# Performance work log

Hardware: AMD Instinct MI355X
Metric: run time of the kernel (lower is better)

Reference implementation:

```python
import jax, jax.numpy as jnp
import numpy as np

N = 100000   # nodes
E = 1600000  # edges
B = 256      # graphs
EPS = 1e-5   # batchnorm eps


def setup_inputs() -> dict:
    key = jax.random.key(0)
    ks = jax.random.split(key, 20)
    inp = {
        "x": jax.random.normal(ks[0], (N, 22), dtype=jnp.float32),
        "edge_index": jax.random.randint(ks[1], (2, E), 0, N, dtype=jnp.int64),
        "batch": jnp.sort(jax.random.randint(ks[2], (N,), 0, B, dtype=jnp.int64)),
        # GCNConv weights (x @ W + b convention)
        "W1": jax.random.normal(ks[3], (22, 64), dtype=jnp.float32) * 0.2,
        "b1": jnp.zeros((64,), dtype=jnp.float32),
        "W2": jax.random.normal(ks[4], (64, 64), dtype=jnp.float32) * 0.12,
        "b2": jnp.zeros((64,), dtype=jnp.float32),
        "W3": jax.random.normal(ks[5], (64, 128), dtype=jnp.float32) * 0.12,
        "b3": jnp.zeros((128,), dtype=jnp.float32),
        # BatchNorm1d params + running stats (eval mode)
        "g1": jax.random.uniform(ks[6], (64,), minval=0.5, maxval=1.5),
        "be1": jax.random.normal(ks[7], (64,)) * 0.1,
        "m1": jax.random.normal(ks[8], (64,)) * 0.1,
        "v1": jax.random.uniform(ks[9], (64,), minval=0.5, maxval=1.5),
        "g2": jax.random.uniform(ks[10], (64,), minval=0.5, maxval=1.5),
        "be2": jax.random.normal(ks[11], (64,)) * 0.1,
        "m2": jax.random.normal(ks[12], (64,)) * 0.1,
        "v2": jax.random.uniform(ks[13], (64,), minval=0.5, maxval=1.5),
    }
    return inp


def _gcn_conv(h, W, b, src, dst, norm_e, dinv):
    # PyG GCNConv: h' = D^{-1/2}(A+I)D^{-1/2} (h W) + b
    h = h @ W                                             # [N, F]
    msg = h[src] * norm_e[:, None]                        # gather + scale [E, F]
    agg = jax.ops.segment_sum(msg, dst, num_segments=N)   # scatter-add
    agg = agg + h * dinv[:, None]                         # self-loop term
    return agg + b


def _bn_eval(x, g, be, m, v):
    return (x - m) * jax.lax.rsqrt(v + EPS) * g + be


def reference(x, edge_index, batch, W1, b1, W2, b2, W3, b3,
              g1, be1, m1, v1, g2, be2, m2, v2):
    src, dst = edge_index[0], edge_index[1]
    # degree with self-loops (computed on target nodes, symmetric norm)
    deg = jax.ops.segment_sum(jnp.ones((E,), x.dtype), dst, num_segments=N) + 1.0
    dis = jax.lax.rsqrt(deg)            # deg^{-1/2}, deg >= 1
    norm_e = dis[src] * dis[dst]        # per-edge norm
    dinv = dis * dis                    # 1/deg for self-loop edges

    h = jax.nn.relu(_bn_eval(_gcn_conv(x, W1, b1, src, dst, norm_e, dinv), g1, be1, m1, v1))
    h = jax.nn.relu(_bn_eval(_gcn_conv(h, W2, b2, src, dst, norm_e, dinv), g2, be2, m2, v2))
    h = jax.nn.relu(_gcn_conv(h, W3, b3, src, dst, norm_e, dinv))

    # global mean pool over graph ids
    sums = jax.ops.segment_sum(h, batch, num_segments=B)              # [B, 128]
    cnts = jax.ops.segment_sum(jnp.ones((N,), h.dtype), batch, num_segments=B)
    return sums / jnp.maximum(cnts, 1.0)[:, None]
```

## Files before the change

### kernel.cpp

```cpp
#include <hip/hip_runtime.h>

#define BN_EPS 1e-5f

typedef _Float16 half_t;
typedef _Float16 half4 __attribute__((ext_vector_type(4)));
typedef _Float16 half8 __attribute__((ext_vector_type(8)));
typedef unsigned int u32;
typedef unsigned short u16;

__device__ __forceinline__ float norm_of(u32 w) {
    u16 hb = (u16)(w & 0x7fffu);
    return (float)__builtin_bit_cast(half_t, hb);
}


#define EPB 4096

__global__ void k_bhist(const int* __restrict__ dst, int* __restrict__ countsT,
                        int nblk, int e) {
    __shared__ int h[256];
    h[threadIdx.x] = 0;
    __syncthreads();
    int base = blockIdx.x * EPB;
    int end = min(base + EPB, e);
    for (int i = base + threadIdx.x; i < end; i += 256)
        atomicAdd(&h[dst[i] >> 9], 1);
    __syncthreads();
    countsT[threadIdx.x * nblk + blockIdx.x] = h[threadIdx.x];
}

__global__ void k_colscan(int* __restrict__ countsT, int* __restrict__ colSum, int nblk) {
    __shared__ int lds[256];
    int t = threadIdx.x;
    int* col = countsT + (size_t)blockIdx.x * nblk;
    int carry = 0;
    for (int base = 0; base < nblk; base += 512) {
        int i0 = base + t * 2, i1 = i0 + 1;
        int v0 = (i0 < nblk) ? col[i0] : 0;
        int v1 = (i1 < nblk) ? col[i1] : 0;
        int s = v0 + v1;
        int val = s;
        lds[t] = val;
        __syncthreads();
        for (int off = 1; off < 256; off <<= 1) {
            int tmp = (t >= off) ? lds[t - off] : 0;
            __syncthreads();
            val += tmp;
            lds[t] = val;
            __syncthreads();
        }
        int run = carry + val - s;
        if (i0 < nblk) col[i0] = run;
        if (i1 < nblk) col[i1] = run + v0;
        carry += lds[255];
        __syncthreads();
    }
    if (t == 0) colSum[blockIdx.x] = carry;
}

__global__ void k_bscatter(const int* __restrict__ src, const int* __restrict__ dst,
                           const int* __restrict__ countsT, const int* __restrict__ colSum,
                           u32* __restrict__ rec, int nblk, int e) {
    __shared__ int lds[256];
    __shared__ int cur[256];
    int t = threadIdx.x;
    int s = colSum[t];
    int val = s;
    lds[t] = val;
    __syncthreads();
    for (int off = 1; off < 256; off <<= 1) {
        int tmp = (t >= off) ? lds[t - off] : 0;
        __syncthreads();
        val += tmp;
        lds[t] = val;
        __syncthreads();
    }
    int basev = val - s;
    cur[t] = countsT[t * nblk + blockIdx.x] + basev;
    __syncthreads();
    int base = blockIdx.x * EPB;
    int end = min(base + EPB, e);
    for (int i = base + t; i < end; i += 256) {
        int d = dst[i], sv = src[i];
        int pos = atomicAdd(&cur[d >> 9], 1);
        rec[pos] = ((u32)sv << 9) | (u32)(d & 511);
    }
}

__global__ void k_bmake1(const u32* __restrict__ rec, const int* __restrict__ colSum,
                         int* __restrict__ rowptr, float* __restrict__ dis,
                         float* __restrict__ dinv, int n) {
    __shared__ int h[512];
    __shared__ int ps[256];
    int t = threadIdx.x;
    int cs = colSum[t];
    int val = cs;
    ps[t] = val;
    __syncthreads();
    for (int off = 1; off < 256; off <<= 1) {
        int tmp = (t >= off) ? ps[t - off] : 0;
        __syncthreads();
        val += tmp;
        ps[t] = val;
        __syncthreads();
    }
    int beg = (blockIdx.x == 0) ? 0 : ps[blockIdx.x - 1];
    int end = ps[blockIdx.x];
    __syncthreads();
    h[t] = 0; h[t + 256] = 0;
    __syncthreads();
    for (int i = beg + t; i < end; i += 256)
        atomicAdd(&h[rec[i] & 511], 1);
    __syncthreads();
    int node0 = blockIdx.x << 9;
    int d0 = h[2 * t], d1 = h[2 * t + 1];
    int pair = d0 + d1;
    ps[t] = pair;
    __syncthreads();
    int val2 = pair;
    for (int off = 1; off < 256; off <<= 1) {
        int tmp = (t >= off) ? ps[t - off] : 0;
        __syncthreads();
        val2 += tmp;
        ps[t] = val2;
        __syncthreads();
    }
    int excl0 = beg + val2 - pair;
    int nodeA = node0 + 2 * t, nodeB = nodeA + 1;
    if (nodeA <= n) rowptr[nodeA] = excl0;
    if (nodeB <= n) rowptr[nodeB] = excl0 + d0;
    if (nodeA < n) { float dd = (float)(d0 + 1); dis[nodeA] = rsqrtf(dd); dinv[nodeA] = 1.0f / dd; }
    if (nodeB < n) { float dd = (float)(d1 + 1); dis[nodeB] = rsqrtf(dd); dinv[nodeB] = 1.0f / dd; }
    if ((n & 511) == 0 && blockIdx.x == gridDim.x - 1 && t == 255) rowptr[n] = end;
}

__global__ void k_bfill(const u32* __restrict__ rec, const int* __restrict__ colSum,
                        const int* __restrict__ rowptr, const float* __restrict__ dis,
                        u32* __restrict__ csr, int n) {
    __shared__ int ps[256];
    __shared__ int cur[512];
    __shared__ float disl[512];
    int t = threadIdx.x;
    int cs = colSum[t];
    int val = cs;
    ps[t] = val;
    __syncthreads();
    for (int off = 1; off < 256; off <<= 1) {
        int tmp = (t >= off) ? ps[t - off] : 0;
        __syncthreads();
        val += tmp;
        ps[t] = val;
        __syncthreads();
    }
    int beg = (blockIdx.x == 0) ? 0 : ps[blockIdx.x - 1];
    int end = ps[blockIdx.x];
    __syncthreads();
    int node0 = blockIdx.x << 9;
    for (int j = t; j < 512; j += 256) {
        int node = node0 + j;
        cur[j]  = (node < n) ? rowptr[node] : 0;
        disl[j] = (node < n) ? dis[node] : 0.0f;
    }
    __syncthreads();
    for (int i = beg + t; i < end; i += 256) {
        u32 r = rec[i];
        int dl = r & 511;
        int s = (int)(r >> 9);
        int pos = atomicAdd(&cur[dl], 1);
        half_t hh = (half_t)(dis[s] * disl[dl]);
        csr[pos] = ((u32)s << 15) | (u32)__builtin_bit_cast(u16, hh);
    }
}


__global__ void k_x2h(const float* __restrict__ X, half_t* __restrict__ Xh, int n) {
    int i = blockIdx.x * blockDim.x + threadIdx.x;
    if (i >= n * 24) return;
    int node = i / 24, c = i % 24;
    Xh[i] = (c < 22) ? (half_t)X[(size_t)node * 22 + c] : (half_t)0.0f;
}


__global__ void k_gather22h(const half_t* __restrict__ Xh, const int* __restrict__ rowptr,
                            const u32* __restrict__ csr, const float* __restrict__ dinv,
                            half_t* __restrict__ out, int n) {
    int node = blockIdx.x * 4 + (threadIdx.x >> 6);
    if (node >= n) return;
    int lane = threadIdx.x & 63;
    int esub = lane >> 3;
    int sub  = lane & 7;
    bool act = sub < 6;
    const half4* X4 = (const half4*)Xh;
    int beg = rowptr[node], end = rowptr[node + 1];
    float4 a0 = make_float4(0, 0, 0, 0), a1 = a0;
    for (int e = beg; e < end; e += 16) {
        int i0 = e + esub, i1 = e + 8 + esub;
        u32 w0 = csr[min(i0, end - 1)];
        u32 w1 = csr[min(i1, end - 1)];
        if (act && i0 < end) {
            float nn = norm_of(w0);
            half4 h = X4[(size_t)(w0 >> 15) * 6 + sub];
            a0.x = fmaf((float)h.x, nn, a0.x); a0.y = fmaf((float)h.y, nn, a0.y);
            a0.z = fmaf((float)h.z, nn, a0.z); a0.w = fmaf((float)h.w, nn, a0.w);
        }
        if (act && i1 < end) {
            float nn = norm_of(w1);
            half4 h = X4[(size_t)(w1 >> 15) * 6 + sub];
            a1.x = fmaf((float)h.x, nn, a1.x); a1.y = fmaf((float)h.y, nn, a1.y);
            a1.z = fmaf((float)h.z, nn, a1.z); a1.w = fmaf((float)h.w, nn, a1.w);
        }
    }
    float4 a;
    a.x = a0.x + a1.x; a.y = a0.y + a1.y; a.z = a0.z + a1.z; a.w = a0.w + a1.w;
#pragma unroll
    for (int d = 8; d <= 32; d <<= 1) {
        a.x += __shfl_xor(a.x, d); a.y += __shfl_xor(a.y, d);
        a.z += __shfl_xor(a.z, d); a.w += __shfl_xor(a.w, d);
    }
    if (esub == 0 && act) {
        float di = dinv[node];
        half4 hs = X4[(size_t)node * 6 + sub];
        half4 r;
        r.x = (half_t)fmaf((float)hs.x, di, a.x);
        r.y = (half_t)fmaf((float)hs.y, di, a.y);
        r.z = (half_t)fmaf((float)hs.z, di, a.z);
        r.w = (half_t)fmaf((float)hs.w, di, a.w);
        ((half4*)out)[(size_t)node * 6 + sub] = r;
    }
}

__global__ void k_gather64h(const half_t* __restrict__ H, const int* __restrict__ rowptr,
                            const u32* __restrict__ csr, const float* __restrict__ dinv,
                            half_t* __restrict__ out, int n) {
    int lane = threadIdx.x & 63;
    int nsub = lane >> 5;
    int hl   = lane & 31;
    int esub = hl >> 3;
    int sub  = hl & 7;
    int node = blockIdx.x * 8 + (int)(threadIdx.x >> 6) * 2 + nsub;
    if (node >= n) return;
    const half8* H8 = (const half8*)H;
    int beg = rowptr[node], end = rowptr[node + 1];
    float a0[8], a1[8];
#pragma unroll
    for (int j = 0; j < 8; ++j) { a0[j] = 0.0f; a1[j] = 0.0f; }
    for (int e = beg; e < end; e += 8) {
        int i0 = e + esub, i1 = e + 4 + esub;
        u32 w0 = csr[min(i0, end - 1)];
        u32 w1 = csr[min(i1, end - 1)];
        if (i0 < end) {
            float nn = norm_of(w0);
            half8 h = H8[(size_t)(w0 >> 15) * 8 + sub];
#pragma unroll
            for (int j = 0; j < 8; ++j) a0[j] = fmaf((float)h[j], nn, a0[j]);
        }
        if (i1 < end) {
            float nn = norm_of(w1);
            half8 h = H8[(size_t)(w1 >> 15) * 8 + sub];
#pragma unroll
            for (int j = 0; j < 8; ++j) a1[j] = fmaf((float)h[j], nn, a1[j]);
        }
    }
    float acc[8];
#pragma unroll
    for (int j = 0; j < 8; ++j) acc[j] = a0[j] + a1[j];
#pragma unroll
    for (int d = 8; d <= 16; d <<= 1) {
#pragma unroll
        for (int j = 0; j < 8; ++j) acc[j] += __shfl_xor(acc[j], d);
    }
    if (esub == 0) {
        float di = dinv[node];
        half8 hs = H8[(size_t)node * 8 + sub];
        half8 r;
#pragma unroll
        for (int j = 0; j < 8; ++j) r[j] = (half_t)fmaf((float)hs[j], di, acc[j]);
        ((half8*)out)[(size_t)node * 8 + sub] = r;
    }
}


__global__ void k_prep_all(const float* __restrict__ W1, const float* __restrict__ b1,
                           const float* __restrict__ g1, const float* __restrict__ be1,
                           const float* __restrict__ m1, const float* __restrict__ v1,
                           const float* __restrict__ W2, const float* __restrict__ b2,
                           const float* __restrict__ g2, const float* __restrict__ be2,
                           const float* __restrict__ m2, const float* __restrict__ v2,
                           const float* __restrict__ W3, const float* __restrict__ b3,
                           float* __restrict__ Wp1, float* __restrict__ C1,
                           float* __restrict__ Wp2, float* __restrict__ C2,
                           float* __restrict__ Wp3, float* __restrict__ C3) {
    int i = blockIdx.x * blockDim.x + threadIdx.x;
    if (i < 24 * 64) {
        int r = i / 64, c = i % 64;
        float A = g1[c] * rsqrtf(v1[c] + BN_EPS);
        Wp1[i] = (r < 22) ? W1[r * 64 + c] * A : 0.0f;
        if (i < 64) C1[i] = be1[i] + (b1[i] - m1[i]) * A;
    }
    int j = i - 24 * 64;
    if (j >= 0 && j < 64 * 64) {
        int c = j % 64;
        float A = g2[c] * rsqrtf(v2[c] + BN_EPS);
        Wp2[j] = W2[j] * A;
        if (j < 64) C2[j] = be2[j] + (b2[j] - m2[j]) * A;
    }
    int k = i - 24 * 64 - 64 * 64;
    if (k >= 0 && k < 64 * 128) {
        Wp3[k] = W3[k];
        if (k < 128) C3[k] = b3[k];
    }
}


template <int FIN, int FOUT>
__global__ __launch_bounds__(256) void k_gemm2(const half_t* __restrict__ P,
                                               const float* __restrict__ Wp,
                                               const float* __restrict__ Cf,
                                               half_t* __restrict__ outp, int n) {
    constexpr int COLS = FOUT / 4;
    int lane = threadIdx.x & 63;
    int part = __builtin_amdgcn_readfirstlane(threadIdx.x >> 6);
    int node = blockIdx.x * 64 + lane;
    if (node >= n) return;

    half8 xr[FIN / 8];
    const half8* p8 = (const half8*)(P + (size_t)node * FIN);
#pragma unroll
    for (int i = 0; i < FIN / 8; ++i) xr[i] = p8[i];
    const half_t* x = (const half_t*)xr;

    const float* wq = Wp + part * COLS;
    const float* cq = Cf + part * COLS;

#pragma unroll 1
    for (int c0 = 0; c0 < COLS; c0 += 16) {
        float4 a0 = make_float4(0, 0, 0, 0), a1 = a0, a2 = a0, a3 = a0;
        const float* wbase = wq + c0;
#pragma unroll
        for (int k = 0; k < FIN; ++k) {
            float xv = (float)x[k];
            const float4* wr = (const float4*)(wbase + k * FOUT);
            float4 w0 = wr[0], w1 = wr[1], w2 = wr[2], w3 = wr[3];
            a0.x = fmaf(xv, w0.x, a0.x); a0.y = fmaf(xv, w0.y, a0.y);
            a0.z = fmaf(xv, w0.z, a0.z); a0.w = fmaf(xv, w0.w, a0.w);
            a1.x = fmaf(xv, w1.x, a1.x); a1.y = fmaf(xv, w1.y, a1.y);
            a1.z = fmaf(xv, w1.z, a1.z); a1.w = fmaf(xv, w1.w, a1.w);
            a2.x = fmaf(xv, w2.x, a2.x); a2.y = fmaf(xv, w2.y, a2.y);
            a2.z = fmaf(xv, w2.z, a2.z); a2.w = fmaf(xv, w2.w, a2.w);
            a3.x = fmaf(xv, w3.x, a3.x); a3.y = fmaf(xv, w3.y, a3.y);
            a3.z = fmaf(xv, w3.z, a3.z); a3.w = fmaf(xv, w3.w, a3.w);
        }
        const float4* c4 = (const float4*)(cq + c0);
        float4 cA = c4[0], cB = c4[1], cC = c4[2], cD = c4[3];
        half8 h0, h1;
        h0[0] = (half_t)fmaxf(a0.x + cA.x, 0.0f); h0[1] = (half_t)fmaxf(a0.y + cA.y, 0.0f);
        h0[2] = (half_t)fmaxf(a0.z + cA.z, 0.0f); h0[3] = (half_t)fmaxf(a0.w + cA.w, 0.0f);
        h0[4] = (half_t)fmaxf(a1.x + cB.x, 0.0f); h0[5] = (half_t)fmaxf(a1.y + cB.y, 0.0f);
        h0[6] = (half_t)fmaxf(a1.z + cB.z, 0.0f); h0[7] = (half_t)fmaxf(a1.w + cB.w, 0.0f);
        h1[0] = (half_t)fmaxf(a2.x + cC.x, 0.0f); h1[1] = (half_t)fmaxf(a2.y + cC.y, 0.0f);
        h1[2] = (half_t)fmaxf(a2.z + cC.z, 0.0f); h1[3] = (half_t)fmaxf(a2.w + cC.w, 0.0f);
        h1[4] = (half_t)fmaxf(a3.x + cD.x, 0.0f); h1[5] = (half_t)fmaxf(a3.y + cD.y, 0.0f);
        h1[6] = (half_t)fmaxf(a3.z + cD.z, 0.0f); h1[7] = (half_t)fmaxf(a3.w + cD.w, 0.0f);
        half8* oh = (half8*)(outp + (size_t)node * FOUT + part * COLS + c0);
        oh[0] = h0;
        oh[1] = h1;
    }
}


__global__ __launch_bounds__(256) void k_gemm3pool(const half_t* __restrict__ P,
                                                   const float* __restrict__ Wp,
                                                   const float* __restrict__ Cf,
                                                   const int* __restrict__ batch,
                                                   float* __restrict__ sums, int n) {
    constexpr int FIN = 64, FOUT = 128, COLS = 32;
    __shared__ half_t tile[128][66];
    __shared__ int batl[64];
    int lane = threadIdx.x & 63;
    int part = __builtin_amdgcn_readfirstlane(threadIdx.x >> 6);
    int node = blockIdx.x * 64 + lane;
    bool valid = node < n;

    if (threadIdx.x < 64) {
        int nd = blockIdx.x * 64 + threadIdx.x;
        batl[threadIdx.x] = (nd < n) ? batch[nd] : -1;
    }

    half8 xr[FIN / 8];
    if (valid) {
        const half8* p8 = (const half8*)(P + (size_t)node * FIN);
#pragma unroll
        for (int i = 0; i < FIN / 8; ++i) xr[i] = p8[i];
    } else {
#pragma unroll
        for (int i = 0; i < FIN / 8; ++i) xr[i] = half8{};
    }
    const half_t* x = (const half_t*)xr;
    const float* wq = Wp + part * COLS;
    const float* cq = Cf + part * COLS;

#pragma unroll 1
    for (int c0 = 0; c0 < COLS; c0 += 16) {
        float4 a0 = make_float4(0, 0, 0, 0), a1 = a0, a2 = a0, a3 = a0;
        const float* wbase = wq + c0;
#pragma unroll
        for (int k = 0; k < FIN; ++k) {
            float xv = (float)x[k];
            const float4* wr = (const float4*)(wbase + k * FOUT);
            float4 w0 = wr[0], w1 = wr[1], w2 = wr[2], w3 = wr[3];
            a0.x = fmaf(xv, w0.x, a0.x); a0.y = fmaf(xv, w0.y, a0.y);
            a0.z = fmaf(xv, w0.z, a0.z); a0.w = fmaf(xv, w0.w, a0.w);
            a1.x = fmaf(xv, w1.x, a1.x); a1.y = fmaf(xv, w1.y, a1.y);
            a1.z = fmaf(xv, w1.z, a1.z); a1.w = fmaf(xv, w1.w, a1.w);
            a2.x = fmaf(xv, w2.x, a2.x); a2.y = fmaf(xv, w2.y, a2.y);
            a2.z = fmaf(xv, w2.z, a2.z); a2.w = fmaf(xv, w2.w, a2.w);
            a3.x = fmaf(xv, w3.x, a3.x); a3.y = fmaf(xv, w3.y, a3.y);
            a3.z = fmaf(xv, w3.z, a3.z); a3.w = fmaf(xv, w3.w, a3.w);
        }
        const float4* c4 = (const float4*)(cq + c0);
        float4 cA = c4[0], cB = c4[1], cC = c4[2], cD = c4[3];
        int r0 = part * COLS + c0;
        tile[r0 +  0][lane] = (half_t)fmaxf(a0.x + cA.x, 0.0f);
        tile[r0 +  1][lane] = (half_t)fmaxf(a0.y + cA.y, 0.0f);
        tile[r0 +  2][lane] = (half_t)fmaxf(a0.z + cA.z, 0.0f);
        tile[r0 +  3][lane] = (half_t)fmaxf(a0.w + cA.w, 0.0f);
        tile[r0 +  4][lane] = (half_t)fmaxf(a1.x + cB.x, 0.0f);
        tile[r0 +  5][lane] = (half_t)fmaxf(a1.y + cB.y, 0.0f);
        tile[r0 +  6][lane] = (half_t)fmaxf(a1.z + cB.z, 0.0f);
        tile[r0 +  7][lane] = (half_t)fmaxf(a1.w + cB.w, 0.0f);
        tile[r0 +  8][lane] = (half_t)fmaxf(a2.x + cC.x, 0.0f);
        tile[r0 +  9][lane] = (half_t)fmaxf(a2.y + cC.y, 0.0f);
        tile[r0 + 10][lane] = (half_t)fmaxf(a2.z + cC.z, 0.0f);
        tile[r0 + 11][lane] = (half_t)fmaxf(a2.w + cC.w, 0.0f);
        tile[r0 + 12][lane] = (half_t)fmaxf(a3.x + cD.x, 0.0f);
        tile[r0 + 13][lane] = (half_t)fmaxf(a3.y + cD.y, 0.0f);
        tile[r0 + 14][lane] = (half_t)fmaxf(a3.z + cD.z, 0.0f);
        tile[r0 + 15][lane] = (half_t)fmaxf(a3.w + cD.w, 0.0f);
    }
    __syncthreads();
    if (threadIdx.x < 128) {
        int col = threadIdx.x;
        int cur = batl[0];
        float acc = 0.0f;
        for (int i = 0; i < 64; ++i) {
            int b = batl[i];
            if (b < 0) break;
            if (b != cur) { atomicAdd(&sums[cur * 128 + col], acc); acc = 0.0f; cur = b; }
            acc += (float)tile[col][i];
        }
        if (cur >= 0) atomicAdd(&sums[cur * 128 + col], acc);
    }
}

__global__ void k_pool_div(const float* __restrict__ sums, const int* __restrict__ batch,
                           float* __restrict__ out, int n, int nB) {
    int i = blockIdx.x * blockDim.x + threadIdx.x;
    if (i >= nB * 128) return;
    int b = i >> 7;
    int lo = 0, hi = n;
    while (lo < hi) { int mid = (lo + hi) >> 1; if (batch[mid] < b) lo = mid + 1; else hi = mid; }
    int start = lo;
    lo = 0; hi = n;
    while (lo < hi) { int mid = (lo + hi) >> 1; if (batch[mid] < b + 1) lo = mid + 1; else hi = mid; }
    float cnt = (float)(lo - start);
    out[i] = sums[i] / fmaxf(cnt, 1.0f);
}


extern "C" void kernel_launch(void* const* d_in, const int* in_sizes, int n_in,
                              void* d_out, int out_size, void* d_ws, size_t ws_size,
                              hipStream_t stream) {
    const float* x   = (const float*)d_in[0];
    const int*   ei  = (const int*)d_in[1];
    const int*   bat = (const int*)d_in[2];
    const float* W1  = (const float*)d_in[3];
    const float* b1  = (const float*)d_in[4];
    const float* W2  = (const float*)d_in[5];
    const float* b2  = (const float*)d_in[6];
    const float* W3  = (const float*)d_in[7];
    const float* b3  = (const float*)d_in[8];
    const float* g1  = (const float*)d_in[9];
    const float* be1 = (const float*)d_in[10];
    const float* m1  = (const float*)d_in[11];
    const float* v1  = (const float*)d_in[12];
    const float* g2  = (const float*)d_in[13];
    const float* be2 = (const float*)d_in[14];
    const float* m2  = (const float*)d_in[15];
    const float* v2  = (const float*)d_in[16];

    const int N = in_sizes[0] / 22;
    const int E = in_sizes[1] / 2;
    const int B = out_size / 128;
    const int* src = ei;
    const int* dst = ei + E;

    const int nblk = (E + EPB - 1) / EPB;
    const int NBKT = (N + 511) >> 9;

    size_t off = 0;
    char* base = (char*)d_ws;
    auto alloc = [&](size_t bytes) -> void* {
        void* p = base + off;
        off = (off + bytes + 255) & ~(size_t)255;
        return p;
    };
    int*    rowptr = (int*)alloc((size_t)(N + 1) * 4);
    int*    countsT = (int*)alloc((size_t)nblk * 256 * 4);
    int*    colSum = (int*)alloc(256 * 4);
    u32*    rec    = (u32*)alloc((size_t)E * 4);
    float*  dis    = (float*)alloc((size_t)N * 4);
    float*  dinv   = (float*)alloc((size_t)N * 4);
    u32*    csr    = (u32*)alloc((size_t)E * 4);
    half_t* Xh     = (half_t*)alloc((size_t)N * 24 * 2);
    half_t* Hh1    = (half_t*)alloc((size_t)N * 64 * 2);
    half_t* Hh2    = (half_t*)alloc((size_t)N * 64 * 2);
    half_t* aggH   = (half_t*)alloc((size_t)N * 64 * 2);
    float*  sums   = (float*)alloc((size_t)B * 128 * 4);
    float*  Wp1    = (float*)alloc(24 * 64 * 4);
    float*  Wp2    = (float*)alloc(64 * 64 * 4);
    float*  Wp3    = (float*)alloc(64 * 128 * 4);
    float*  C1     = (float*)alloc(64 * 4);
    float*  C2     = (float*)alloc(64 * 4);
    float*  C3     = (float*)alloc(128 * 4);

    const int T = 256;
    auto blk = [](long long n, int t) { return (int)((n + t - 1) / t); };

    k_prep_all<<<blk(24 * 64 + 64 * 64 + 64 * 128, T), T, 0, stream>>>(
        W1, b1, g1, be1, m1, v1, W2, b2, g2, be2, m2, v2, W3, b3,
        Wp1, C1, Wp2, C2, Wp3, C3);

    k_bhist<<<nblk, T, 0, stream>>>(dst, countsT, nblk, E);
    k_colscan<<<256, T, 0, stream>>>(countsT, colSum, nblk);
    k_bscatter<<<nblk, T, 0, stream>>>(src, dst, countsT, colSum, rec, nblk, E);
    k_bmake1<<<NBKT, T, 0, stream>>>(rec, colSum, rowptr, dis, dinv, N);
    k_bfill<<<NBKT, T, 0, stream>>>(rec, colSum, rowptr, dis, csr, N);

    k_x2h<<<blk((long long)N * 24, T), T, 0, stream>>>(x, Xh, N);

    k_gather22h<<<blk(N, 4), T, 0, stream>>>(Xh, rowptr, csr, dinv, aggH, N);
    k_gemm2<24, 64><<<blk(N, 64), T, 0, stream>>>(aggH, Wp1, C1, Hh1, N);

    k_gather64h<<<blk(N, 8), T, 0, stream>>>(Hh1, rowptr, csr, dinv, aggH, N);
    k_gemm2<64, 64><<<blk(N, 64), T, 0, stream>>>(aggH, Wp2, C2, Hh2, N);

    k_gather64h<<<blk(N, 8), T, 0, stream>>>(Hh2, rowptr, csr, dinv, aggH, N);
    hipMemsetAsync(sums, 0, (size_t)B * 128 * sizeof(float), stream);
    k_gemm3pool<<<blk(N, 64), T, 0, stream>>>(aggH, Wp3, C3, bat, sums, N);

    k_pool_div<<<blk(B * 128, T), T, 0, stream>>>(sums, bat, (float*)d_out, N, B);
}
```

Before: 338.8 us.

## Fuse aggregation with GEMM per layer and build CSR in fixed-capacity buckets

```diff
diff --git a/kernel.cpp b/kernel.cpp
--- a/kernel.cpp
+++ b/kernel.cpp
@@ -1,8 +1,11 @@
 #include <hip/hip_runtime.h>
 
 #define BN_EPS 1e-5f
+#define EPB 4096
+#define CAP 10240
 
 typedef _Float16 half_t;
+typedef _Float16 half2v __attribute__((ext_vector_type(2)));
 typedef _Float16 half4 __attribute__((ext_vector_type(4)));
 typedef _Float16 half8 __attribute__((ext_vector_type(8)));
 typedef unsigned int u32;
@@ -14,89 +17,93 @@
 }
 
 
-#define EPB 4096
-
-__global__ void k_bhist(const int* __restrict__ dst, int* __restrict__ countsT,
-                        int nblk, int e) {
+__global__ void k_front(const float* __restrict__ X, half_t* __restrict__ Xh,
+                        const float* __restrict__ W1, const float* __restrict__ b1,
+                        const float* __restrict__ g1, const float* __restrict__ be1,
+                        const float* __restrict__ m1, const float* __restrict__ v1,
+                        const float* __restrict__ W2, const float* __restrict__ b2,
+                        const float* __restrict__ g2, const float* __restrict__ be2,
+                        const float* __restrict__ m2, const float* __restrict__ v2,
+                        const float* __restrict__ W3, const float* __restrict__ b3,
+                        float* __restrict__ Wp1, float* __restrict__ C1,
+                        float* __restrict__ Wp2, float* __restrict__ C2,
+                        float* __restrict__ Wp3, float* __restrict__ C3,
+                        int* __restrict__ gcnt, float* __restrict__ sums,
+                        int n, int nB) {
+    int i = blockIdx.x * 256 + threadIdx.x;
+    if (i < 24 * 64) {
+        int r = i / 64, c = i % 64;
+        float A = g1[c] * rsqrtf(v1[c] + BN_EPS);
+        Wp1[i] = (r < 22) ? W1[r * 64 + c] * A : 0.0f;
+        if (i < 64) C1[i] = be1[i] + (b1[i] - m1[i]) * A;
+    } else if (i < 24 * 64 + 64 * 64) {
+        int j = i - 24 * 64;
+        int c = j % 64;
+        float A = g2[c] * rsqrtf(v2[c] + BN_EPS);
+        Wp2[j] = W2[j] * A;
+        if (j < 64) C2[j] = be2[j] + (b2[j] - m2[j]) * A;
+    } else if (i < 24 * 64 + 64 * 64 + 64 * 128) {
+        int k = i - 24 * 64 - 64 * 64;
+        Wp3[k] = W3[k];
+        if (k < 128) C3[k] = b3[k];
+    }
+    if (i < 256) gcnt[i] = 0;
+    if (i < nB * 128) sums[i] = 0.0f;
+    if ((long long)i < (long long)n * 24) {
+        int node = i / 24, c = i % 24;
+        Xh[i] = (c < 22) ? (half_t)X[(size_t)node * 22 + c] : (half_t)0.0f;
+    }
+}
+
+
+__global__ __launch_bounds__(256) void k_scatter(const int* __restrict__ src,
+                                                 const int* __restrict__ dst,
+                                                 int* __restrict__ gcnt,
+                                                 u32* __restrict__ rec, int e) {
     __shared__ int h[256];
-    h[threadIdx.x] = 0;
+    __shared__ int cur[256];
+    int t = threadIdx.x;
+    h[t] = 0;
     __syncthreads();
     int base = blockIdx.x * EPB;
     int end = min(base + EPB, e);
-    for (int i = base + threadIdx.x; i < end; i += 256)
+    for (int i = base + t; i < end; i += 256)
         atomicAdd(&h[dst[i] >> 9], 1);
     __syncthreads();
-    countsT[threadIdx.x * nblk + blockIdx.x] = h[threadIdx.x];
-}
-
-__global__ void k_colscan(int* __restrict__ countsT, int* __restrict__ colSum, int nblk) {
-    __shared__ int lds[256];
-    int t = threadIdx.x;
-    int* col = countsT + (size_t)blockIdx.x * nblk;
-    int carry = 0;
-    for (int base = 0; base < nblk; base += 512) {
-        int i0 = base + t * 2, i1 = i0 + 1;
-        int v0 = (i0 < nblk) ? col[i0] : 0;
-        int v1 = (i1 < nblk) ? col[i1] : 0;
-        int s = v0 + v1;
-        int val = s;
-        lds[t] = val;
-        __syncthreads();
-        for (int off = 1; off < 256; off <<= 1) {
-            int tmp = (t >= off) ? lds[t - off] : 0;
-            __syncthreads();
-            val += tmp;
-            lds[t] = val;
-            __syncthreads();
-        }
-        int run = carry + val - s;
-        if (i0 < nblk) col[i0] = run;
-        if (i1 < nblk) col[i1] = run + v0;
-        carry += lds[255];
-        __syncthreads();
-    }
-    if (t == 0) colSum[blockIdx.x] = carry;
-}
-
-__global__ void k_bscatter(const int* __restrict__ src, const int* __restrict__ dst,
-                           const int* __restrict__ countsT, const int* __restrict__ colSum,
-                           u32* __restrict__ rec, int nblk, int e) {
-    __shared__ int lds[256];
-    __shared__ int cur[256];
-    int t = threadIdx.x;
-    int s = colSum[t];
-    int val = s;
-    lds[t] = val;
-    __syncthreads();
-    for (int off = 1; off < 256; off <<= 1) {
-        int tmp = (t >= off) ? lds[t - off] : 0;
-        __syncthreads();
-        val += tmp;
-        lds[t] = val;
-        __syncthreads();
-    }
-    int basev = val - s;
-    cur[t] = countsT[t * nblk + blockIdx.x] + basev;
-    __syncthreads();
-    int base = blockIdx.x * EPB;
-    int end = min(base + EPB, e);
+    int c = h[t];
+    cur[t] = (c > 0) ? atomicAdd(&gcnt[t], c) : 0;
+    __syncthreads();
     for (int i = base + t; i < end; i += 256) {
         int d = dst[i], sv = src[i];
-        int pos = atomicAdd(&cur[d >> 9], 1);
-        rec[pos] = ((u32)sv << 9) | (u32)(d & 511);
-    }
-}
-
-__global__ void k_bmake1(const u32* __restrict__ rec, const int* __restrict__ colSum,
-                         int* __restrict__ rowptr, float* __restrict__ dis,
-                         float* __restrict__ dinv, int n) {
+        int bk = d >> 9;
+        int pos = atomicAdd(&cur[bk], 1);
+        if (pos < CAP)
+            rec[(size_t)bk * CAP + pos] = ((u32)sv << 9) | (u32)(d & 511);
+    }
+}
+
+
+__global__ __launch_bounds__(256) void k_bmake(const u32* __restrict__ rec,
+                                               const int* __restrict__ gcnt,
+                                               int2* __restrict__ rp,
+                                               float* __restrict__ dis,
+                                               float* __restrict__ dinv, int n) {
     __shared__ int h[512];
     __shared__ int ps[256];
     int t = threadIdx.x;
-    int cs = colSum[t];
-    int val = cs;
-    ps[t] = val;
-    __syncthreads();
+    int b = blockIdx.x;
+    int cnt = min(gcnt[b], CAP);
+    size_t beg = (size_t)b * CAP;
+    h[t] = 0; h[t + 256] = 0;
+    __syncthreads();
+    for (int i = t; i < cnt; i += 256)
+        atomicAdd(&h[rec[beg + i] & 511], 1);
+    __syncthreads();
+    int d0 = h[2 * t], d1 = h[2 * t + 1];
+    int pair = d0 + d1;
+    ps[t] = pair;
+    __syncthreads();
+    int val = pair;
     for (int off = 1; off < 256; off <<= 1) {
         int tmp = (t >= off) ? ps[t - off] : 0;
         __syncthreads();
@@ -104,66 +111,44 @@
         ps[t] = val;
         __syncthreads();
     }
-    int beg = (blockIdx.x == 0) ? 0 : ps[blockIdx.x - 1];
-    int end = ps[blockIdx.x];
-    __syncthreads();
-    h[t] = 0; h[t + 256] = 0;
-    __syncthreads();
-    for (int i = beg + t; i < end; i += 256)
-        atomicAdd(&h[rec[i] & 511], 1);
-    __syncthreads();
-    int node0 = blockIdx.x << 9;
-    int d0 = h[2 * t], d1 = h[2 * t + 1];
-    int pair = d0 + d1;
-    ps[t] = pair;
-    __syncthreads();
-    int val2 = pair;
-    for (int off = 1; off < 256; off <<= 1) {
-        int tmp = (t >= off) ? ps[t - off] : 0;
-        __syncthreads();
-        val2 += tmp;
-        ps[t] = val2;
-        __syncthreads();
-    }
-    int excl0 = beg + val2 - pair;
+    int excl = (int)beg + val - pair;
+    int node0 = b << 9;
     int nodeA = node0 + 2 * t, nodeB = nodeA + 1;
-    if (nodeA <= n) rowptr[nodeA] = excl0;
-    if (nodeB <= n) rowptr[nodeB] = excl0 + d0;
-    if (nodeA < n) { float dd = (float)(d0 + 1); dis[nodeA] = rsqrtf(dd); dinv[nodeA] = 1.0f / dd; }
-    if (nodeB < n) { float dd = (float)(d1 + 1); dis[nodeB] = rsqrtf(dd); dinv[nodeB] = 1.0f / dd; }
-    if ((n & 511) == 0 && blockIdx.x == gridDim.x - 1 && t == 255) rowptr[n] = end;
-}
-
-__global__ void k_bfill(const u32* __restrict__ rec, const int* __restrict__ colSum,
-                        const int* __restrict__ rowptr, const float* __restrict__ dis,
-                        u32* __restrict__ csr, int n) {
-    __shared__ int ps[256];
+    if (nodeA < n) {
+        rp[nodeA] = make_int2(excl, excl + d0);
+        float dd = (float)(d0 + 1);
+        dis[nodeA] = rsqrtf(dd);
+        dinv[nodeA] = 1.0f / dd;
+    }
+    if (nodeB < n) {
+        rp[nodeB] = make_int2(excl + d0, excl + d0 + d1);
+        float dd = (float)(d1 + 1);
+        dis[nodeB] = rsqrtf(dd);
+        dinv[nodeB] = 1.0f / dd;
+    }
+}
+
+
+__global__ __launch_bounds__(256) void k_bfill(const u32* __restrict__ rec,
+                                               const int* __restrict__ gcnt,
+                                               const int2* __restrict__ rp,
+                                               const float* __restrict__ dis,
+                                               u32* __restrict__ csr, int n) {
     __shared__ int cur[512];
     __shared__ float disl[512];
     int t = threadIdx.x;
-    int cs = colSum[t];
-    int val = cs;
-    ps[t] = val;
-    __syncthreads();
-    for (int off = 1; off < 256; off <<= 1) {
-        int tmp = (t >= off) ? ps[t - off] : 0;
-        __syncthreads();
-        val += tmp;
-        ps[t] = val;
-        __syncthreads();
-    }
-    int beg = (blockIdx.x == 0) ? 0 : ps[blockIdx.x - 1];
-    int end = ps[blockIdx.x];
-    __syncthreads();
-    int node0 = blockIdx.x << 9;
+    int b = blockIdx.x;
+    int cnt = min(gcnt[b], CAP);
+    size_t beg = (size_t)b * CAP;
+    int node0 = b << 9;
     for (int j = t; j < 512; j += 256) {
         int node = node0 + j;
-        cur[j]  = (node < n) ? rowptr[node] : 0;
+        cur[j] = (node < n) ? rp[node].x : 0;
         disl[j] = (node < n) ? dis[node] : 0.0f;
     }
     __syncthreads();
-    for (int i = beg + t; i < end; i += 256) {
-        u32 r = rec[i];
+    for (int i = t; i < cnt; i += 256) {
+        u32 r = rec[beg + i];
         int dl = r & 511;
         int s = (int)(r >> 9);
         int pos = atomicAdd(&cur[dl], 1);
@@ -173,284 +158,239 @@
 }
 
 
-__global__ void k_x2h(const float* __restrict__ X, half_t* __restrict__ Xh, int n) {
-    int i = blockIdx.x * blockDim.x + threadIdx.x;
-    if (i >= n * 24) return;
-    int node = i / 24, c = i % 24;
-    Xh[i] = (c < 22) ? (half_t)X[(size_t)node * 22 + c] : (half_t)0.0f;
-}
-
-
-__global__ void k_gather22h(const half_t* __restrict__ Xh, const int* __restrict__ rowptr,
-                            const u32* __restrict__ csr, const float* __restrict__ dinv,
-                            half_t* __restrict__ out, int n) {
-    int node = blockIdx.x * 4 + (threadIdx.x >> 6);
-    if (node >= n) return;
-    int lane = threadIdx.x & 63;
+__device__ __forceinline__ void gather64_to_tile(const half_t* __restrict__ H,
+                                                 const int2* __restrict__ rp,
+                                                 const u32* __restrict__ csr,
+                                                 const float* __restrict__ dinv,
+                                                 float* tilerow, int node, int n,
+                                                 int lane) {
+    int hl = lane & 31;
+    int esub = hl >> 3;
+    int sub = hl & 7;
+    if (node < n) {
+        const half8* H8 = (const half8*)H;
+        int2 be = rp[node];
+        int beg = be.x, end = be.y;
+        float a0[8], a1[8];
+#pragma unroll
+        for (int j = 0; j < 8; ++j) { a0[j] = 0.0f; a1[j] = 0.0f; }
+        for (int e = beg; e < end; e += 8) {
+            int i0 = e + esub, i1 = e + 4 + esub;
+            u32 w0 = csr[min(i0, end - 1)];
+            u32 w1 = csr[min(i1, end - 1)];
+            if (i0 < end) {
+                float nn = norm_of(w0);
+                half8 h = H8[(size_t)(w0 >> 15) * 8 + sub];
+#pragma unroll
+                for (int j = 0; j < 8; ++j) a0[j] = fmaf((float)h[j], nn, a0[j]);
+            }
+            if (i1 < end) {
+                float nn = norm_of(w1);
+                half8 h = H8[(size_t)(w1 >> 15) * 8 + sub];
+#pragma unroll
+                for (int j = 0; j < 8; ++j) a1[j] = fmaf((float)h[j], nn, a1[j]);
+            }
+        }
+        float acc[8];
+#pragma unroll
+        for (int j = 0; j < 8; ++j) acc[j] = a0[j] + a1[j];
+#pragma unroll
+        for (int d = 8; d <= 16; d <<= 1) {
+#pragma unroll
+            for (int j = 0; j < 8; ++j) acc[j] += __shfl_xor(acc[j], d);
+        }
+        if (esub == 0) {
+            float di = dinv[node];
+            half8 hs = H8[(size_t)node * 8 + sub];
+            float4 r0, r1;
+            r0.x = fmaf((float)hs[0], di, acc[0]);
+            r0.y = fmaf((float)hs[1], di, acc[1]);
+            r0.z = fmaf((float)hs[2], di, acc[2]);
+            r0.w = fmaf((float)hs[3], di, acc[3]);
+            r1.x = fmaf((float)hs[4], di, acc[4]);
+            r1.y = fmaf((float)hs[5], di, acc[5]);
+            r1.z = fmaf((float)hs[6], di, acc[6]);
+            r1.w = fmaf((float)hs[7], di, acc[7]);
+            *(float4*)(tilerow + sub * 8) = r0;
+            *(float4*)(tilerow + sub * 8 + 4) = r1;
+        }
+    }
+}
+
+
+__global__ __launch_bounds__(256) void k_l1(const half_t* __restrict__ Xh,
+                                            const int2* __restrict__ rp,
+                                            const u32* __restrict__ csr,
+                                            const float* __restrict__ dinv,
+                                            const float* __restrict__ Wp1,
+                                            const float* __restrict__ C1,
+                                            half_t* __restrict__ Hh1, int n) {
+    __shared__ __align__(16) float tile[4][24];
+    int tid = threadIdx.x;
+    int wave = tid >> 6, lane = tid & 63;
+    int node = blockIdx.x * 4 + wave;
     int esub = lane >> 3;
-    int sub  = lane & 7;
+    int sub = lane & 7;
     bool act = sub < 6;
-    const half4* X4 = (const half4*)Xh;
-    int beg = rowptr[node], end = rowptr[node + 1];
-    float4 a0 = make_float4(0, 0, 0, 0), a1 = a0;
-    for (int e = beg; e < end; e += 16) {
-        int i0 = e + esub, i1 = e + 8 + esub;
-        u32 w0 = csr[min(i0, end - 1)];
-        u32 w1 = csr[min(i1, end - 1)];
-        if (act && i0 < end) {
-            float nn = norm_of(w0);
-            half4 h = X4[(size_t)(w0 >> 15) * 6 + sub];
-            a0.x = fmaf((float)h.x, nn, a0.x); a0.y = fmaf((float)h.y, nn, a0.y);
-            a0.z = fmaf((float)h.z, nn, a0.z); a0.w = fmaf((float)h.w, nn, a0.w);
-        }
-        if (act && i1 < end) {
-            float nn = norm_of(w1);
-            half4 h = X4[(size_t)(w1 >> 15) * 6 + sub];
-            a1.x = fmaf((float)h.x, nn, a1.x); a1.y = fmaf((float)h.y, nn, a1.y);
-            a1.z = fmaf((float)h.z, nn, a1.z); a1.w = fmaf((float)h.w, nn, a1.w);
-        }
-    }
-    float4 a;
-    a.x = a0.x + a1.x; a.y = a0.y + a1.y; a.z = a0.z + a1.z; a.w = a0.w + a1.w;
-#pragma unroll
-    for (int d = 8; d <= 32; d <<= 1) {
-        a.x += __shfl_xor(a.x, d); a.y += __shfl_xor(a.y, d);
-        a.z += __shfl_xor(a.z, d); a.w += __shfl_xor(a.w, d);
-    }
-    if (esub == 0 && act) {
-        float di = dinv[node];
-        half4 hs = X4[(size_t)node * 6 + sub];
-        half4 r;
-        r.x = (half_t)fmaf((float)hs.x, di, a.x);
-        r.y = (half_t)fmaf((float)hs.y, di, a.y);
-        r.z = (half_t)fmaf((float)hs.z, di, a.z);
-        r.w = (half_t)fmaf((float)hs.w, di, a.w);
-        ((half4*)out)[(size_t)node * 6 + sub] = r;
-    }
-}
-
-__global__ void k_gather64h(const half_t* __restrict__ H, const int* __restrict__ rowptr,
-                            const u32* __restrict__ csr, const float* __restrict__ dinv,
-                            half_t* __restrict__ out, int n) {
-    int lane = threadIdx.x & 63;
+    if (node < n) {
+        const half4* X4 = (const half4*)Xh;
+        int2 be = rp[node];
+        int beg = be.x, end = be.y;
+        float4 a0 = make_float4(0, 0, 0, 0), a1 = a0;
+        for (int e = beg; e < end; e += 16) {
+            int i0 = e + esub, i1 = e + 8 + esub;
+            u32 w0 = csr[min(i0, end - 1)];
+            u32 w1 = csr[min(i1, end - 1)];
+            if (act && i0 < end) {
+                float nn = norm_of(w0);
+                half4 h = X4[(size_t)(w0 >> 15) * 6 + sub];
+                a0.x = fmaf((float)h.x, nn, a0.x); a0.y = fmaf((float)h.y, nn, a0.y);
+                a0.z = fmaf((float)h.z, nn, a0.z); a0.w = fmaf((float)h.w, nn, a0.w);
+            }
+            if (act && i1 < end) {
+                float nn = norm_of(w1);
+                half4 h = X4[(size_t)(w1 >> 15) * 6 + sub];
+                a1.x = fmaf((float)h.x, nn, a1.x); a1.y = fmaf((float)h.y, nn, a1.y);
+                a1.z = fmaf((float)h.z, nn, a1.z); a1.w = fmaf((float)h.w, nn, a1.w);
+            }
+        }
+        float4 a;
+        a.x = a0.x + a1.x; a.y = a0.y + a1.y; a.z = a0.z + a1.z; a.w = a0.w + a1.w;
+#pragma unroll
+        for (int d = 8; d <= 32; d <<= 1) {
+            a.x += __shfl_xor(a.x, d); a.y += __shfl_xor(a.y, d);
+            a.z += __shfl_xor(a.z, d); a.w += __shfl_xor(a.w, d);
+        }
+        if (esub == 0 && act) {
+            float di = dinv[node];
+            half4 hs = X4[(size_t)node * 6 + sub];
+            float4 r;
+            r.x = fmaf((float)hs.x, di, a.x);
+            r.y = fmaf((float)hs.y, di, a.y);
+            r.z = fmaf((float)hs.z, di, a.z);
+            r.w = fmaf((float)hs.w, di, a.w);
+            *(float4*)&tile[wave][sub * 4] = r;
+        }
+    }
+    __syncthreads();
+    if (node < n) {
+        int col = lane;
+        float acc = C1[col];
+#pragma unroll
+        for (int k = 0; k < 24; ++k)
+            acc = fmaf(tile[wave][k], Wp1[k * 64 + col], acc);
+        Hh1[(size_t)node * 64 + col] = (half_t)fmaxf(acc, 0.0f);
+    }
+}
+
+
+__global__ __launch_bounds__(256) void k_l2(const half_t* __restrict__ H,
+                                            const int2* __restrict__ rp,
+                                            const u32* __restrict__ csr,
+                                            const float* __restrict__ dinv,
+                                            const float* __restrict__ Wp2,
+                                            const float* __restrict__ C2,
+                                            half_t* __restrict__ Ho, int n) {
+    __shared__ __align__(16) float tile[8][64];
+    int tid = threadIdx.x;
+    int lane = tid & 63;
     int nsub = lane >> 5;
-    int hl   = lane & 31;
-    int esub = hl >> 3;
-    int sub  = hl & 7;
-    int node = blockIdx.x * 8 + (int)(threadIdx.x >> 6) * 2 + nsub;
-    if (node >= n) return;
-    const half8* H8 = (const half8*)H;
-    int beg = rowptr[node], end = rowptr[node + 1];
-    float a0[8], a1[8];
-#pragma unroll
-    for (int j = 0; j < 8; ++j) { a0[j] = 0.0f; a1[j] = 0.0f; }
-    for (int e = beg; e < end; e += 8) {
-        int i0 = e + esub, i1 = e + 4 + esub;
-        u32 w0 = csr[min(i0, end - 1)];
-        u32 w1 = csr[min(i1, end - 1)];
-        if (i0 < end) {
-            float nn = norm_of(w0);
-            half8 h = H8[(size_t)(w0 >> 15) * 8 + sub];
-#pragma unroll
-            for (int j = 0; j < 8; ++j) a0[j] = fmaf((float)h[j], nn, a0[j]);
-        }
-        if (i1 < end) {
-            float nn = norm_of(w1);
-            half8 h = H8[(size_t)(w1 >> 15) * 8 + sub];
-#pragma unroll
-            for (int j = 0; j < 8; ++j) a1[j] = fmaf((float)h[j], nn, a1[j]);
-        }
-    }
-    float acc[8];
-#pragma unroll
-    for (int j = 0; j < 8; ++j) acc[j] = a0[j] + a1[j];
-#pragma unroll
-    for (int d = 8; d <= 16; d <<= 1) {
-#pragma unroll
-        for (int j = 0; j < 8; ++j) acc[j] += __shfl_xor(acc[j], d);
-    }
-    if (esub == 0) {
-        float di = dinv[node];
-        half8 hs = H8[(size_t)node * 8 + sub];
-        half8 r;
-#pragma unroll
-        for (int j = 0; j < 8; ++j) r[j] = (half_t)fmaf((float)hs[j], di, acc[j]);
-        ((half8*)out)[(size_t)node * 8 + sub] = r;
-    }
-}
-
-
-__global__ void k_prep_all(const float* __restrict__ W1, const float* __restrict__ b1,
-                           const float* __restrict__ g1, const float* __restrict__ be1,
-                           const float* __restrict__ m1, const float* __restrict__ v1,
-                           const float* __restrict__ W2, const float* __restrict__ b2,
-                           const float* __restrict__ g2, const float* __restrict__ be2,
-                           const float* __restrict__ m2, const float* __restrict__ v2,
-                           const float* __restrict__ W3, const float* __restrict__ b3,
-                           float* __restrict__ Wp1, float* __restrict__ C1,
-                           float* __restrict__ Wp2, float* __restrict__ C2,
-                           float* __restrict__ Wp3, float* __restrict__ C3) {
-    int i = blockIdx.x * blockDim.x + threadIdx.x;
-    if (i < 24 * 64) {
-        int r = i / 64, c = i % 64;
-        float A = g1[c] * rsqrtf(v1[c] + BN_EPS);
-        Wp1[i] = (r < 22) ? W1[r * 64 + c] * A : 0.0f;
-        if (i < 64) C1[i] = be1[i] + (b1[i] - m1[i]) * A;
-    }
-    int j = i - 24 * 64;
-    if (j >= 0 && j < 64 * 64) {
-        int c = j % 64;
-        float A = g2[c] * rsqrtf(v2[c] + BN_EPS);
-        Wp2[j] = W2[j] * A;
-        if (j < 64) C2[j] = be2[j] + (b2[j] - m2[j]) * A;
-    }
-    int k = i - 24 * 64 - 64 * 64;
-    if (k >= 0 && k < 64 * 128) {
-        Wp3[k] = W3[k];
-        if (k < 128) C3[k] = b3[k];
-    }
-}
-
-
-template <int FIN, int FOUT>
-__global__ __launch_bounds__(256) void k_gemm2(const half_t* __restrict__ P,
-                                               const float* __restrict__ Wp,
-                                               const float* __restrict__ Cf,
-                                               half_t* __restrict__ outp, int n) {
-    constexpr int COLS = FOUT / 4;
-    int lane = threadIdx.x & 63;
-    int part = __builtin_amdgcn_readfirstlane(threadIdx.x >> 6);
-    int node = blockIdx.x * 64 + lane;
-    if (node >= n) return;
-
-    half8 xr[FIN / 8];
-    const half8* p8 = (const half8*)(P + (size_t)node * FIN);
-#pragma unroll
-    for (int i = 0; i < FIN / 8; ++i) xr[i] = p8[i];
-    const half_t* x = (const half_t*)xr;
-
-    const float* wq = Wp + part * COLS;
-    const float* cq = Cf + part * COLS;
-
-#pragma unroll 1
-    for (int c0 = 0; c0 < COLS; c0 += 16) {
-        float4 a0 = make_float4(0, 0, 0, 0), a1 = a0, a2 = a0, a3 = a0;
-        const float* wbase = wq + c0;
-#pragma unroll
-        for (int k = 0; k < FIN; ++k) {
-            float xv = (float)x[k];
-            const float4* wr = (const float4*)(wbase + k * FOUT);
-            float4 w0 = wr[0], w1 = wr[1], w2 = wr[2], w3 = wr[3];
-            a0.x = fmaf(xv, w0.x, a0.x); a0.y = fmaf(xv, w0.y, a0.y);
-            a0.z = fmaf(xv, w0.z, a0.z); a0.w = fmaf(xv, w0.w, a0.w);
-            a1.x = fmaf(xv, w1.x, a1.x); a1.y = fmaf(xv, w1.y, a1.y);
-            a1.z = fmaf(xv, w1.z, a1.z); a1.w = fmaf(xv, w1.w, a1.w);
-            a2.x = fmaf(xv, w2.x, a2.x); a2.y = fmaf(xv, w2.y, a2.y);
-            a2.z = fmaf(xv, w2.z, a2.z); a2.w = fmaf(xv, w2.w, a2.w);
-            a3.x = fmaf(xv, w3.x, a3.x); a3.y = fmaf(xv, w3.y, a3.y);
-            a3.z = fmaf(xv, w3.z, a3.z); a3.w = fmaf(xv, w3.w, a3.w);
-        }
-        const float4* c4 = (const float4*)(cq + c0);
-        float4 cA = c4[0], cB = c4[1], cC = c4[2], cD = c4[3];
-        half8 h0, h1;
-        h0[0] = (half_t)fmaxf(a0.x + cA.x, 0.0f); h0[1] = (half_t)fmaxf(a0.y + cA.y, 0.0f);
-        h0[2] = (half_t)fmaxf(a0.z + cA.z, 0.0f); h0[3] = (half_t)fmaxf(a0.w + cA.w, 0.0f);
-        h0[4] = (half_t)fmaxf(a1.x + cB.x, 0.0f); h0[5] = (half_t)fmaxf(a1.y + cB.y, 0.0f);
-        h0[6] = (half_t)fmaxf(a1.z + cB.z, 0.0f); h0[7] = (half_t)fmaxf(a1.w + cB.w, 0.0f);
-        h1[0] = (half_t)fmaxf(a2.x + cC.x, 0.0f); h1[1] = (half_t)fmaxf(a2.y + cC.y, 0.0f);
-        h1[2] = (half_t)fmaxf(a2.z + cC.z, 0.0f); h1[3] = (half_t)fmaxf(a2.w + cC.w, 0.0f);
-        h1[4] = (half_t)fmaxf(a3.x + cD.x, 0.0f); h1[5] = (half_t)fmaxf(a3.y + cD.y, 0.0f);
-        h1[6] = (half_t)fmaxf(a3.z + cD.z, 0.0f); h1[7] = (half_t)fmaxf(a3.w + cD.w, 0.0f);
-        half8* oh = (half8*)(outp + (size_t)node * FOUT + part * COLS + c0);
-        oh[0] = h0;
-        oh[1] = h1;
-    }
-}
-
-
-__global__ __launch_bounds__(256) void k_gemm3pool(const half_t* __restrict__ P,
-                                                   const float* __restrict__ Wp,
-                                                   const float* __restrict__ Cf,
-                                                   const int* __restrict__ batch,
-                                                   float* __restrict__ sums, int n) {
-    constexpr int FIN = 64, FOUT = 128, COLS = 32;
-    __shared__ half_t tile[128][66];
-    __shared__ int batl[64];
-    int lane = threadIdx.x & 63;
-    int part = __builtin_amdgcn_readfirstlane(threadIdx.x >> 6);
-    int node = blockIdx.x * 64 + lane;
-    bool valid = node < n;
-
-    if (threadIdx.x < 64) {
-        int nd = blockIdx.x * 64 + threadIdx.x;
-        batl[threadIdx.x] = (nd < n) ? batch[nd] : -1;
-    }
-
-    half8 xr[FIN / 8];
-    if (valid) {
-        const half8* p8 = (const half8*)(P + (size_t)node * FIN);
-#pragma unroll
-        for (int i = 0; i < FIN / 8; ++i) xr[i] = p8[i];
-    } else {
-#pragma unroll
-        for (int i = 0; i < FIN / 8; ++i) xr[i] = half8{};
-    }
-    const half_t* x = (const half_t*)xr;
-    const float* wq = Wp + part * COLS;
-    const float* cq = Cf + part * COLS;
-
-#pragma unroll 1
-    for (int c0 = 0; c0 < COLS; c0 += 16) {
-        float4 a0 = make_float4(0, 0, 0, 0), a1 = a0, a2 = a0, a3 = a0;
-        const float* wbase = wq + c0;
-#pragma unroll
-        for (int k = 0; k < FIN; ++k) {
-            float xv = (float)x[k];
-            const float4* wr = (const float4*)(wbase + k * FOUT);
-            float4 w0 = wr[0], w1 = wr[1], w2 = wr[2], w3 = wr[3];
-            a0.x = fmaf(xv, w0.x, a0.x); a0.y = fmaf(xv, w0.y, a0.y);
-            a0.z = fmaf(xv, w0.z, a0.z); a0.w = fmaf(xv, w0.w, a0.w);
-            a1.x = fmaf(xv, w1.x, a1.x); a1.y = fmaf(xv, w1.y, a1.y);
-            a1.z = fmaf(xv, w1.z, a1.z); a1.w = fmaf(xv, w1.w, a1.w);
-            a2.x = fmaf(xv, w2.x, a2.x); a2.y = fmaf(xv, w2.y, a2.y);
-            a2.z = fmaf(xv, w2.z, a2.z); a2.w = fmaf(xv, w2.w, a2.w);
-            a3.x = fmaf(xv, w3.x, a3.x); a3.y = fmaf(xv, w3.y, a3.y);
-            a3.z = fmaf(xv, w3.z, a3.z); a3.w = fmaf(xv, w3.w, a3.w);
-        }
-        const float4* c4 = (const float4*)(cq + c0);
-        float4 cA = c4[0], cB = c4[1], cC = c4[2], cD = c4[3];
-        int r0 = part * COLS + c0;
-        tile[r0 +  0][lane] = (half_t)fmaxf(a0.x + cA.x, 0.0f);
-        tile[r0 +  1][lane] = (half_t)fmaxf(a0.y + cA.y, 0.0f);
-        tile[r0 +  2][lane] = (half_t)fmaxf(a0.z + cA.z, 0.0f);
-        tile[r0 +  3][lane] = (half_t)fmaxf(a0.w + cA.w, 0.0f);
-        tile[r0 +  4][lane] = (half_t)fmaxf(a1.x + cB.x, 0.0f);
-        tile[r0 +  5][lane] = (half_t)fmaxf(a1.y + cB.y, 0.0f);
-        tile[r0 +  6][lane] = (half_t)fmaxf(a1.z + cB.z, 0.0f);
-        tile[r0 +  7][lane] = (half_t)fmaxf(a1.w + cB.w, 0.0f);
-        tile[r0 +  8][lane] = (half_t)fmaxf(a2.x + cC.x, 0.0f);
-        tile[r0 +  9][lane] = (half_t)fmaxf(a2.y + cC.y, 0.0f);
-        tile[r0 + 10][lane] = (half_t)fmaxf(a2.z + cC.z, 0.0f);
-        tile[r0 + 11][lane] = (half_t)fmaxf(a2.w + cC.w, 0.0f);
-        tile[r0 + 12][lane] = (half_t)fmaxf(a3.x + cD.x, 0.0f);
-        tile[r0 + 13][lane] = (half_t)fmaxf(a3.y + cD.y, 0.0f);
-        tile[r0 + 14][lane] = (half_t)fmaxf(a3.z + cD.z, 0.0f);
-        tile[r0 + 15][lane] = (half_t)fmaxf(a3.w + cD.w, 0.0f);
-    }
-    __syncthreads();
-    if (threadIdx.x < 128) {
-        int col = threadIdx.x;
-        int cur = batl[0];
+    int loc = (tid >> 6) * 2 + nsub;
+    int node = blockIdx.x * 8 + loc;
+    gather64_to_tile(H, rp, csr, dinv, &tile[loc][0], node, n, lane);
+    __syncthreads();
+    int nd = tid >> 5;
+    int cp = tid & 31;
+    int gnode = blockIdx.x * 8 + nd;
+    if (gnode < n) {
+        float acc0 = C2[2 * cp], acc1 = C2[2 * cp + 1];
+        const float4* T4 = (const float4*)tile[nd];
+        const float* Wb = Wp2 + 2 * cp;
+#pragma unroll
+        for (int k4 = 0; k4 < 16; ++k4) {
+            float4 x4 = T4[k4];
+            const float* w = Wb + k4 * 4 * 64;
+            float2 wa = *(const float2*)(w);
+            float2 wb = *(const float2*)(w + 64);
+            float2 wc = *(const float2*)(w + 128);
+            float2 wd = *(const float2*)(w + 192);
+            acc0 = fmaf(x4.x, wa.x, acc0); acc1 = fmaf(x4.x, wa.y, acc1);
+            acc0 = fmaf(x4.y, wb.x, acc0); acc1 = fmaf(x4.y, wb.y, acc1);
+            acc0 = fmaf(x4.z, wc.x, acc0); acc1 = fmaf(x4.z, wc.y, acc1);
+            acc0 = fmaf(x4.w, wd.x, acc0); acc1 = fmaf(x4.w, wd.y, acc1);
+        }
+        half2v hv;
+        hv[0] = (half_t)fmaxf(acc0, 0.0f);
+        hv[1] = (half_t)fmaxf(acc1, 0.0f);
+        *(half2v*)(Ho + (size_t)gnode * 64 + 2 * cp) = hv;
+    }
+}
+
+
+__global__ __launch_bounds__(512) void k_l3(const half_t* __restrict__ H,
+                                            const int2* __restrict__ rp,
+                                            const u32* __restrict__ csr,
+                                            const float* __restrict__ dinv,
+                                            const float* __restrict__ Wp3,
+                                            const float* __restrict__ C3,
+                                            const int* __restrict__ batch,
+                                            float* __restrict__ sums, int n) {
+    __shared__ __align__(16) float tile[16][64];
+    __shared__ __align__(16) float ot[16][128];
+    __shared__ int batl[16];
+    int tid = threadIdx.x;
+    if (tid < 16) {
+        int nd0 = blockIdx.x * 16 + tid;
+        batl[tid] = (nd0 < n) ? batch[nd0] : -1;
+    }
+    int lane = tid & 63;
+    int nsub = lane >> 5;
+    int loc = (tid >> 6) * 2 + nsub;
+    int node = blockIdx.x * 16 + loc;
+    gather64_to_tile(H, rp, csr, dinv, &tile[loc][0], node, n, lane);
+    __syncthreads();
+    int nd = tid >> 5;
+    int cp = tid & 31;
+    if (blockIdx.x * 16 + nd < n) {
+        float4 acc = ((const float4*)C3)[cp];
+        const float4* T4 = (const float4*)tile[nd];
+#pragma unroll
+        for (int k4 = 0; k4 < 16; ++k4) {
+            float4 x4 = T4[k4];
+            const float4* w = (const float4*)(Wp3 + (k4 * 4) * 128) + cp;
+            float4 w0 = w[0], w1 = w[32], w2 = w[64], w3 = w[96];
+            acc.x = fmaf(x4.x, w0.x, acc.x); acc.y = fmaf(x4.x, w0.y, acc.y);
+            acc.z = fmaf(x4.x, w0.z, acc.z); acc.w = fmaf(x4.x, w0.w, acc.w);
+            acc.x = fmaf(x4.y, w1.x, acc.x); acc.y = fmaf(x4.y, w1.y, acc.y);
+            acc.z = fmaf(x4.y, w1.z, acc.z); acc.w = fmaf(x4.y, w1.w, acc.w);
+            acc.x = fmaf(x4.z, w2.x, acc.x); acc.y = fmaf(x4.z, w2.y, acc.y);
+            acc.z = fmaf(x4.z, w2.z, acc.z); acc.w = fmaf(x4.z, w2.w, acc.w);
+            acc.x = fmaf(x4.w, w3.x, acc.x); acc.y = fmaf(x4.w, w3.y, acc.y);
+            acc.z = fmaf(x4.w, w3.z, acc.z); acc.w = fmaf(x4.w, w3.w, acc.w);
+        }
+        acc.x = fmaxf(acc.x, 0.0f); acc.y = fmaxf(acc.y, 0.0f);
+        acc.z = fmaxf(acc.z, 0.0f); acc.w = fmaxf(acc.w, 0.0f);
+        *(float4*)&ot[nd][4 * cp] = acc;
+    }
+    __syncthreads();
+    if (tid < 128) {
+        int col = tid;
         float acc = 0.0f;
-        for (int i = 0; i < 64; ++i) {
-            int b = batl[i];
+        int cur = -1;
+        for (int i2 = 0; i2 < 16; ++i2) {
+            int b = batl[i2];
             if (b < 0) break;
-            if (b != cur) { atomicAdd(&sums[cur * 128 + col], acc); acc = 0.0f; cur = b; }
-            acc += (float)tile[col][i];
+            if (b != cur) {
+                if (cur >= 0) atomicAdd(&sums[cur * 128 + col], acc);
+                acc = 0.0f;
+                cur = b;
+            }
+            acc += ot[i2][col];
         }
         if (cur >= 0) atomicAdd(&sums[cur * 128 + col], acc);
     }
 }
+
 
 __global__ void k_pool_div(const float* __restrict__ sums, const int* __restrict__ batch,
                            float* __restrict__ out, int n, int nB) {
@@ -504,17 +444,15 @@
         off = (off + bytes + 255) & ~(size_t)255;
         return p;
     };
-    int*    rowptr = (int*)alloc((size_t)(N + 1) * 4);
-    int*    countsT = (int*)alloc((size_t)nblk * 256 * 4);
-    int*    colSum = (int*)alloc(256 * 4);
-    u32*    rec    = (u32*)alloc((size_t)E * 4);
+    int2*   rp     = (int2*)alloc((size_t)N * 8);
+    int*    gcnt   = (int*)alloc(256 * 4);
+    u32*    rec    = (u32*)alloc((size_t)NBKT * CAP * 4);
     float*  dis    = (float*)alloc((size_t)N * 4);
     float*  dinv   = (float*)alloc((size_t)N * 4);
-    u32*    csr    = (u32*)alloc((size_t)E * 4);
+    u32*    csr    = (u32*)alloc((size_t)NBKT * CAP * 4);
     half_t* Xh     = (half_t*)alloc((size_t)N * 24 * 2);
     half_t* Hh1    = (half_t*)alloc((size_t)N * 64 * 2);
     half_t* Hh2    = (half_t*)alloc((size_t)N * 64 * 2);
-    half_t* aggH   = (half_t*)alloc((size_t)N * 64 * 2);
     float*  sums   = (float*)alloc((size_t)B * 128 * 4);
     float*  Wp1    = (float*)alloc(24 * 64 * 4);
     float*  Wp2    = (float*)alloc(64 * 64 * 4);
@@ -526,27 +464,23 @@
     const int T = 256;
     auto blk = [](long long n, int t) { return (int)((n + t - 1) / t); };
 
-    k_prep_all<<<blk(24 * 64 + 64 * 64 + 64 * 128, T), T, 0, stream>>>(
-        W1, b1, g1, be1, m1, v1, W2, b2, g2, be2, m2, v2, W3, b3,
-        Wp1, C1, Wp2, C2, Wp3, C3);
-
-    k_bhist<<<nblk, T, 0, stream>>>(dst, countsT, nblk, E);
-    k_colscan<<<256, T, 0, stream>>>(countsT, colSum, nblk);
-    k_bscatter<<<nblk, T, 0, stream>>>(src, dst, countsT, colSum, rec, nblk, E);
-    k_bmake1<<<NBKT, T, 0, stream>>>(rec, colSum, rowptr, dis, dinv, N);
-    k_bfill<<<NBKT, T, 0, stream>>>(rec, colSum, rowptr, dis, csr, N);
-
-    k_x2h<<<blk((long long)N * 24, T), T, 0, stream>>>(x, Xh, N);
-
-    k_gather22h<<<blk(N, 4), T, 0, stream>>>(Xh, rowptr, csr, dinv, aggH, N);
-    k_gemm2<24, 64><<<blk(N, 64), T, 0, stream>>>(aggH, Wp1, C1, Hh1, N);
-
-    k_gather64h<<<blk(N, 8), T, 0, stream>>>(Hh1, rowptr, csr, dinv, aggH, N);
-    k_gemm2<64, 64><<<blk(N, 64), T, 0, stream>>>(aggH, Wp2, C2, Hh2, N);
-
-    k_gather64h<<<blk(N, 8), T, 0, stream>>>(Hh2, rowptr, csr, dinv, aggH, N);
-    hipMemsetAsync(sums, 0, (size_t)B * 128 * sizeof(float), stream);
-    k_gemm3pool<<<blk(N, 64), T, 0, stream>>>(aggH, Wp3, C3, bat, sums, N);
-
-    k_pool_div<<<blk(B * 128, T), T, 0, stream>>>(sums, bat, (float*)d_out, N, B);
-}
+    int gf = blk((long long)N * 24, T);
+    int gf2 = blk(24 * 64 + 64 * 64 + 64 * 128, T);
+    int gf3 = blk((long long)B * 128, T);
+    if (gf2 > gf) gf = gf2;
+    if (gf3 > gf) gf = gf3;
+
+    k_front<<<gf, T, 0, stream>>>(x, Xh, W1, b1, g1, be1, m1, v1,
+                                  W2, b2, g2, be2, m2, v2, W3, b3,
+                                  Wp1, C1, Wp2, C2, Wp3, C3, gcnt, sums, N, B);
+
+    k_scatter<<<nblk, T, 0, stream>>>(src, dst, gcnt, rec, E);
+    k_bmake<<<NBKT, T, 0, stream>>>(rec, gcnt, rp, dis, dinv, N);
+    k_bfill<<<NBKT, T, 0, stream>>>(rec, gcnt, rp, dis, csr, N);
+
+    k_l1<<<blk(N, 4), T, 0, stream>>>(Xh, rp, csr, dinv, Wp1, C1, Hh1, N);
+    k_l2<<<blk(N, 8), T, 0, stream>>>(Hh1, rp, csr, dinv, Wp2, C2, Hh2, N);
+    k_l3<<<blk(N, 16), 512, 0, stream>>>(Hh2, rp, csr, dinv, Wp3, C3, bat, sums, N);
+
+    k_pool_div<<<blk((long long)B * 128, T), T, 0, stream>>>(sums, bat, (float*)d_out, N, B);
+}
```

Measured after the change: 441.3 us. 1.3x slower.
